# Optimization experiments

Measured on AMD Instinct MI355X. Metric: run time of the kernel, lower is better.

The kernel has to match this reference:

```python
import jax, jax.numpy as jnp
import numpy as np

B, N, D, H = 8, 2048, 512, 8  # batch, seq (incl. CLS), emb_dim, heads


def setup_inputs() -> dict:
    key = jax.random.key(0)
    kx, km, k1, k2, k3, k4 = jax.random.split(key, 6)
    x = jax.random.normal(kx, (B, N, D), dtype=jnp.float32)
    # mask covers the N-1 non-CLS tokens; forward pads a leading True for CLS
    mask = jax.random.bernoulli(km, p=0.9, shape=(B, N - 1))
    s = 0.02
    Wqkv = jax.random.normal(k1, (D, 3 * D), dtype=jnp.float32) * s
    bqkv = jax.random.normal(k2, (3 * D,), dtype=jnp.float32) * s
    Wout = jax.random.normal(k3, (D, D), dtype=jnp.float32) * s
    bout = jax.random.normal(k4, (D,), dtype=jnp.float32) * s
    return {"x": x, "mask": mask, "Wqkv": Wqkv, "bqkv": bqkv,
            "Wout": Wout, "bout": bout, "num_heads": H}


def reference(x, mask, Wqkv, bqkv, Wout, bout, num_heads):
    b, n, d = x.shape
    h = num_heads
    dh = d // h
    scale = d ** (-0.5)  # NOTE: module scales by emb_dim^-0.5, not head_dim^-0.5

    qkv = x @ Wqkv + bqkv                      # [b, n, 3d]
    q, k, v = jnp.split(qkv, 3, axis=-1)
    def to_heads(t):
        return t.reshape(b, n, h, dh).transpose(0, 2, 1, 3)  # [b, h, n, dh]
    q, k, v = map(to_heads, (q, k, v))

    scores = jnp.einsum('bhqd,bhkd->bhqk', q, k) * scale     # [b, h, n, n]

    # pad leading True for CLS token, then outer-product pair mask
    m = jnp.pad(mask, ((0, 0), (1, 0)), constant_values=True)  # [b, n]
    pair = m[:, None, :, None] & m[:, None, None, :]           # [b, 1, n, n]
    neg = jnp.asarray(-1e9, dtype=scores.dtype)  # finite stand-in for -inf (avoids NaN rows)
    scores = jnp.where(pair, scores, neg)

    attn = jax.nn.softmax(scores, axis=-1)
    out = jnp.einsum('bhqk,bhkd->bhqd', attn, v)               # [b, h, n, dh]
    out = out.transpose(0, 2, 1, 3).reshape(b, n, d)
    return out @ Wout + bout
```

## Files before the change

### kernel.cpp

```cpp
#include <hip/hip_runtime.h>
#include <math.h>

#define BB  8
#define SEQ 2048
#define EMB 512
#define NH  8
#define DH  64
#define NBH (BB * NH)
#define MROWS (BB * SEQ)
#define QKV_ELEMS ((size_t)NBH * SEQ * DH)
#define MASK_ELEMS (BB * (SEQ - 1))
#define QSCALE 0.06375871307545f

typedef __attribute__((ext_vector_type(8))) short short8;
typedef __attribute__((ext_vector_type(4))) float float4e;
typedef unsigned short ushort_t;

static __device__ inline unsigned short f2bf(float f) {
    unsigned int u = __float_as_uint(f);
    unsigned int r = (u + 0x7fffu + ((u >> 16) & 1u)) >> 16;
    return (unsigned short)r;
}

static __device__ inline float bf2f(unsigned short h) {
    return __uint_as_float((unsigned int)h << 16);
}

static __device__ inline void gl_lds16(const unsigned short* g, unsigned short* l) {
    __builtin_amdgcn_global_load_lds(
        (const __attribute__((address_space(1))) void*)g,
        (__attribute__((address_space(3))) void*)l, 16, 0, 0);
}

__global__ void decode_mask(const void* __restrict__ mraw, ushort_t* __restrict__ pmh) {
    __shared__ int flag;
    if (threadIdx.x == 0) flag = 0;
    __syncthreads();
    const unsigned int* mi = (const unsigned int*)mraw;
    int local = 0;
    for (int i = threadIdx.x; i < MASK_ELEMS / 4; i += 256) {
        if (mi[i] > 1u) local = 1;
    }
    if (local) flag = 1;
    __syncthreads();
    const int isbyte = flag;
    const unsigned char* mb = (const unsigned char*)mraw;
    const int* m32 = (const int*)mraw;
    for (int i = threadIdx.x; i < BB * SEQ; i += 256) {
        const int b = i >> 11, n = i & (SEQ - 1);
        int v;
        if (n == 0) v = 1;
        else {
            const int src = b * (SEQ - 1) + n - 1;
            v = isbyte ? (int)mb[src] : (m32[src] != 0 ? 1 : 0);
        }
        pmh[i] = v ? 0x3F80 : 0;
    }
}

__global__ __launch_bounds__(256) void conv_x(const float* __restrict__ x,
                                              ushort_t* __restrict__ xb) {
    const size_t i = ((size_t)blockIdx.x * 256 + threadIdx.x) * 4;
    float4 v = *(const float4*)&x[i];
    ushort4 o;
    o.x = f2bf(v.x); o.y = f2bf(v.y); o.z = f2bf(v.z); o.w = f2bf(v.w);
    *(ushort4*)&xb[i] = o;
}

__global__ __launch_bounds__(256) void wtrans(const float* __restrict__ src,
                                              ushort_t* __restrict__ dst,
                                              int K, int N) {
    __shared__ float T[32][33];
    const int tid = threadIdx.x;
    const int n0 = blockIdx.x * 32;
    const int k0 = blockIdx.y * 32;
    {
        const int r = tid >> 3, c4 = (tid & 7) * 4;
        *(float4*)&T[r][c4] = *(const float4*)&src[(size_t)(k0 + r) * N + n0 + c4];
    }
    __syncthreads();
    const int n = tid >> 3, k4 = (tid & 7) * 4;
    ushort4 hv;
    hv.x = f2bf(T[k4 + 0][n]);
    hv.y = f2bf(T[k4 + 1][n]);
    hv.z = f2bf(T[k4 + 2][n]);
    hv.w = f2bf(T[k4 + 3][n]);
    *(ushort4*)&dst[(size_t)(n0 + n) * K + k0 + k4] = hv;
}

__global__ __launch_bounds__(256) void qkv_mfma(const ushort_t* __restrict__ xb,
                                                const ushort_t* __restrict__ wt,
                                                const float* __restrict__ bias,
                                                ushort_t* __restrict__ qb,
                                                ushort_t* __restrict__ kb,
                                                ushort_t* __restrict__ vt) {
    __shared__ __align__(16) ushort_t As[128 * 32];
    __shared__ __align__(16) ushort_t Bs[128 * 32];
    const int tid  = threadIdx.x;
    const int w    = tid >> 6;
    const int lane = tid & 63;
    const int l16  = lane & 15;
    const int quad = lane >> 4;
    const int wq   = w >> 1;
    const int wn   = w & 1;
    const int row0 = blockIdx.y * 128;
    const int col0 = blockIdx.x * 128;

    float4e acc[4][4];
    #pragma unroll
    for (int i = 0; i < 4; ++i)
        #pragma unroll
        for (int j = 0; j < 4; ++j) acc[i][j] = (float4e){0.f, 0.f, 0.f, 0.f};

    const int srow = tid >> 2;
    const int csrc = (tid & 3) ^ (srow & 3);

    for (int k0 = 0; k0 < EMB; k0 += 32) {
        #pragma unroll
        for (int s = 0; s < 2; ++s) {
            const int row = s * 64 + srow;
            gl_lds16(xb + (size_t)(row0 + row) * EMB + k0 + csrc * 8,
                     As + s * 2048 + w * 512);
            gl_lds16(wt + (size_t)(col0 + row) * EMB + k0 + csrc * 8,
                     Bs + s * 2048 + w * 512);
        }
        __syncthreads();
        short8 af[4], bf[4];
        #pragma unroll
        for (int mt = 0; mt < 4; ++mt) {
            const int rm = wq * 64 + mt * 16 + l16;
            af[mt] = *(const short8*)(As + rm * 32 + ((quad ^ (rm & 3)) * 8));
        }
        #pragma unroll
        for (int nt = 0; nt < 4; ++nt) {
            const int rn = wn * 64 + nt * 16 + l16;
            bf[nt] = *(const short8*)(Bs + rn * 32 + ((quad ^ (rn & 3)) * 8));
        }
        #pragma unroll
        for (int mt = 0; mt < 4; ++mt)
            #pragma unroll
            for (int nt = 0; nt < 4; ++nt)
                acc[mt][nt] = __builtin_amdgcn_mfma_f32_16x16x32_bf16(af[mt], bf[nt], acc[mt][nt], 0, 0, 0);
        __syncthreads();
    }

    #pragma unroll
    for (int nt = 0; nt < 4; ++nt) {
        const int cb    = col0 + wn * 64 + nt * 16;
        const int which = cb >> 9;
        const int h     = (cb >> 6) & 7;
        const int dcol  = (cb & 63) + l16;
        const float bz  = bias[cb + l16];
        if (which == 2) {
            #pragma unroll
            for (int mt = 0; mt < 4; ++mt) {
                const int rg = row0 + wq * 64 + mt * 16 + quad * 4;
                const int b = rg >> 11, n = rg & (SEQ - 1);
                ushort4 ov;
                ov.x = f2bf(acc[mt][nt][0] + bz);
                ov.y = f2bf(acc[mt][nt][1] + bz);
                ov.z = f2bf(acc[mt][nt][2] + bz);
                ov.w = f2bf(acc[mt][nt][3] + bz);
                *(ushort4*)&vt[((size_t)(b * NH + h) * DH + dcol) * SEQ + n] = ov;
            }
        } else {
            ushort_t* base = (which == 0) ? qb : kb;
            const float sc = (which == 0) ? QSCALE : 1.0f;
            #pragma unroll
            for (int mt = 0; mt < 4; ++mt) {
                #pragma unroll
                for (int i = 0; i < 4; ++i) {
                    const int rg = row0 + wq * 64 + mt * 16 + quad * 4 + i;
                    const int b = rg >> 11;
                    const int n = rg & (SEQ - 1);
                    base[((size_t)(b * NH + h) * SEQ + n) * DH + dcol] =
                        f2bf((acc[mt][nt][i] + bz) * sc);
                }
            }
        }
    }
}

__global__ __launch_bounds__(256, 4) void attn_mfma(const ushort_t* __restrict__ qb,
                                                    const ushort_t* __restrict__ kb,
                                                    const ushort_t* __restrict__ vt,
                                                    const ushort_t* __restrict__ pmh,
                                                    ushort_t* __restrict__ ab) {
    __shared__ __align__(16) ushort_t Ks[64 * 64];
    __shared__ __align__(16) ushort_t Vts[64 * 64];
    __shared__ __align__(16) ushort_t Ps[4][32 * 64];
    __shared__ ushort_t mskh[SEQ];
    __shared__ float lw[128];

    const int tid  = threadIdx.x;
    const int qt   = blockIdx.x & 15;
    const int bh   = blockIdx.x >> 4;
    const int b    = bh >> 3;
    const int h    = bh & 7;
    const int w    = tid >> 6;
    const int lane = tid & 63;
    const int l16  = lane & 15;
    const int quad = lane >> 4;

    *(short8*)(mskh + tid * 8) = *(const short8*)(pmh + b * SEQ + tid * 8);

    const ushort_t* qbase = qb + ((size_t)bh * SEQ + qt * 128 + w * 32 + l16) * DH;
    short8 qf0[2], qf1[2];
    #pragma unroll
    for (int g = 0; g < 2; ++g) {
        qf0[g] = *(const short8*)(qbase + g * 16 * DH + quad * 8);
        qf1[g] = *(const short8*)(qbase + g * 16 * DH + 32 + quad * 8);
    }

    __syncthreads();

    float mqf[2], fnq[2];
    #pragma unroll
    for (int g = 0; g < 2; ++g) {
        mqf[g] = bf2f(mskh[qt * 128 + w * 32 + g * 16 + l16]);
        fnq[g] = 1.0f - mqf[g];
    }

    float4e o[2][4];
    #pragma unroll
    for (int g = 0; g < 2; ++g)
        #pragma unroll
        for (int d = 0; d < 4; ++d) o[g][d] = (float4e){0.f, 0.f, 0.f, 0.f};
    float l_i[2] = {0.f, 0.f};

    int srow[2], soff[2];
    #pragma unroll
    for (int s = 0; s < 2; ++s) {
        const int c = s * 256 + w * 64 + lane;
        srow[s] = c >> 3;
        soff[s] = ((c & 7) ^ (srow[s] & 7)) * 8;
    }
    const ushort_t* kptr = kb + (size_t)bh * SEQ * DH;
    const ushort_t* vptr = vt + (size_t)bh * DH * SEQ;

    int koff0[4], koff1[4];
    #pragma unroll
    for (int t = 0; t < 4; ++t) {
        const int row = t * 16 + l16;
        koff0[t] = row * 64 + ((quad ^ (row & 7)) * 8);
        koff1[t] = row * 64 + (((4 + quad) ^ (row & 7)) * 8);
    }
    const int psw = (l16 & 7) * 2;
    ushort_t* pwv = &Ps[w][0];
    const int prd0 = ((quad * 2) ^ psw) * 4;
    const int prd1 = (((4 + quad) * 2) ^ psw) * 4;

    for (int kt = 0; kt < 32; ++kt) {
        __syncthreads();
        #pragma unroll
        for (int s = 0; s < 2; ++s) {
            gl_lds16(kptr + (size_t)(kt * 64 + srow[s]) * DH + soff[s],
                     Ks + s * 2048 + w * 512);
            gl_lds16(vptr + (size_t)srow[s] * SEQ + kt * 64 + soff[s],
                     Vts + s * 2048 + w * 512);
        }
        __syncthreads();

        #pragma unroll
        for (int bkb = 0; bkb < 4; ++bkb) {
            const short8 kf0 = *(const short8*)(Ks + koff0[bkb]);
            const short8 kf1 = *(const short8*)(Ks + koff1[bkb]);
            float4e st[2];
            #pragma unroll
            for (int g = 0; g < 2; ++g) {
                st[g] = (float4e){0.f, 0.f, 0.f, 0.f};
                st[g] = __builtin_amdgcn_mfma_f32_16x16x32_bf16(kf0, qf0[g], st[g], 0, 0, 0);
                st[g] = __builtin_amdgcn_mfma_f32_16x16x32_bf16(kf1, qf1[g], st[g], 0, 0, 0);
            }
            const ushort4 mk4 = *(const ushort4*)(mskh + kt * 64 + bkb * 16 + quad * 4);
            const float mkf[4] = {bf2f(mk4.x), bf2f(mk4.y), bf2f(mk4.z), bf2f(mk4.w)};
            const int pc = ((bkb * 4 + quad) ^ psw) * 4;
            #pragma unroll
            for (int g = 0; g < 2; ++g) {
                float p0 = fmaf(__builtin_amdgcn_exp2f(st[g][0]) * mkf[0], mqf[g], fnq[g]);
                float p1 = fmaf(__builtin_amdgcn_exp2f(st[g][1]) * mkf[1], mqf[g], fnq[g]);
                float p2 = fmaf(__builtin_amdgcn_exp2f(st[g][2]) * mkf[2], mqf[g], fnq[g]);
                float p3 = fmaf(__builtin_amdgcn_exp2f(st[g][3]) * mkf[3], mqf[g], fnq[g]);
                l_i[g] += (p0 + p1) + (p2 + p3);
                ushort4 pk;
                pk.x = f2bf(p0); pk.y = f2bf(p1); pk.z = f2bf(p2); pk.w = f2bf(p3);
                *(ushort4*)(pwv + (g * 16 + l16) * 64 + pc) = pk;
            }
        }

        short8 pf0[2], pf1[2];
        #pragma unroll
        for (int g = 0; g < 2; ++g) {
            pf0[g] = *(const short8*)(pwv + (g * 16 + l16) * 64 + prd0);
            pf1[g] = *(const short8*)(pwv + (g * 16 + l16) * 64 + prd1);
        }
        #pragma unroll
        for (int dhb = 0; dhb < 4; ++dhb) {
            const short8 vf0 = *(const short8*)(Vts + koff0[dhb]);
            const short8 vf1 = *(const short8*)(Vts + koff1[dhb]);
            #pragma unroll
            for (int g = 0; g < 2; ++g) {
                o[g][dhb] = __builtin_amdgcn_mfma_f32_16x16x32_bf16(pf0[g], vf0, o[g][dhb], 0, 0, 0);
                o[g][dhb] = __builtin_amdgcn_mfma_f32_16x16x32_bf16(pf1[g], vf1, o[g][dhb], 0, 0, 0);
            }
        }
    }

    #pragma unroll
    for (int g = 0; g < 2; ++g) {
        float l = l_i[g];
        l += __shfl_xor(l, 16);
        l += __shfl_xor(l, 32);
        lw[w * 32 + g * 16 + l16] = l;
    }

    ushort_t* ob = ab + ((size_t)b * SEQ + qt * 128 + w * 32) * EMB + h * DH;
    #pragma unroll
    for (int g = 0; g < 2; ++g) {
        #pragma unroll
        for (int i = 0; i < 4; ++i) {
            const int row = g * 16 + quad * 4 + i;
            const float inv = 1.0f / lw[w * 32 + row];
            #pragma unroll
            for (int dhb = 0; dhb < 4; ++dhb)
                ob[(size_t)row * EMB + dhb * 16 + l16] = f2bf(o[g][dhb][i] * inv);
        }
    }
}

__global__ __launch_bounds__(256) void out_mfma(const ushort_t* __restrict__ ab,
                                                const ushort_t* __restrict__ wot,
                                                const float* __restrict__ bias,
                                                float* __restrict__ out) {
    __shared__ __align__(16) ushort_t As[128 * 32];
    __shared__ __align__(16) ushort_t Bs[128 * 32];
    const int tid  = threadIdx.x;
    const int w    = tid >> 6;
    const int lane = tid & 63;
    const int l16  = lane & 15;
    const int quad = lane >> 4;
    const int wq   = w >> 1;
    const int wn   = w & 1;
    const int row0 = blockIdx.y * 128;
    const int col0 = blockIdx.x * 128;

    float4e acc[4][4];
    #pragma unroll
    for (int i = 0; i < 4; ++i)
        #pragma unroll
        for (int j = 0; j < 4; ++j) acc[i][j] = (float4e){0.f, 0.f, 0.f, 0.f};

    const int srow = tid >> 2;
    const int csrc = (tid & 3) ^ (srow & 3);

    for (int k0 = 0; k0 < EMB; k0 += 32) {
        #pragma unroll
        for (int s = 0; s < 2; ++s) {
            const int row = s * 64 + srow;
            gl_lds16(ab + (size_t)(row0 + row) * EMB + k0 + csrc * 8,
                     As + s * 2048 + w * 512);
            gl_lds16(wot + (size_t)(col0 + row) * EMB + k0 + csrc * 8,
                     Bs + s * 2048 + w * 512);
        }
        __syncthreads();
        short8 af[4], bf[4];
        #pragma unroll
        for (int mt = 0; mt < 4; ++mt) {
            const int rm = wq * 64 + mt * 16 + l16;
            af[mt] = *(const short8*)(As + rm * 32 + ((quad ^ (rm & 3)) * 8));
        }
        #pragma unroll
        for (int nt = 0; nt < 4; ++nt) {
            const int rn = wn * 64 + nt * 16 + l16;
            bf[nt] = *(const short8*)(Bs + rn * 32 + ((quad ^ (rn & 3)) * 8));
        }
        #pragma unroll
        for (int mt = 0; mt < 4; ++mt)
            #pragma unroll
            for (int nt = 0; nt < 4; ++nt)
                acc[mt][nt] = __builtin_amdgcn_mfma_f32_16x16x32_bf16(af[mt], bf[nt], acc[mt][nt], 0, 0, 0);
        __syncthreads();
    }

    #pragma unroll
    for (int nt = 0; nt < 4; ++nt) {
        const int col_g = col0 + wn * 64 + nt * 16 + l16;
        const float bz = bias[col_g];
        #pragma unroll
        for (int mt = 0; mt < 4; ++mt) {
            #pragma unroll
            for (int i = 0; i < 4; ++i) {
                const int row_g = row0 + wq * 64 + mt * 16 + quad * 4 + i;
                out[(size_t)row_g * EMB + col_g] = acc[mt][nt][i] + bz;
            }
        }
    }
}

extern "C" void kernel_launch(void* const* d_in, const int* in_sizes, int n_in,
                              void* d_out, int out_size, void* d_ws, size_t ws_size,
                              hipStream_t stream) {
    const float* x    = (const float*)d_in[0];
    const void*  mask = d_in[1];
    const float* Wqkv = (const float*)d_in[2];
    const float* bqkv = (const float*)d_in[3];
    const float* Wout = (const float*)d_in[4];
    const float* bout = (const float*)d_in[5];
    float* out = (float*)d_out;

    ushort_t* xb  = (ushort_t*)d_ws;
    ushort_t* wqt = xb + (size_t)MROWS * EMB;
    ushort_t* wot = wqt + (size_t)1536 * EMB;
    ushort_t* qb  = wot + (size_t)EMB * EMB;
    ushort_t* kb  = qb + QKV_ELEMS;
    ushort_t* vt  = kb + QKV_ELEMS;
    ushort_t* ab  = vt + QKV_ELEMS;
    ushort_t* pmh = ab + (size_t)MROWS * EMB;

    decode_mask<<<1, 256, 0, stream>>>(mask, pmh);
    conv_x<<<dim3(MROWS * EMB / 1024), 256, 0, stream>>>(x, xb);
    wtrans<<<dim3(1536 / 32, EMB / 32), 256, 0, stream>>>(Wqkv, wqt, EMB, 1536);
    wtrans<<<dim3(EMB / 32, EMB / 32), 256, 0, stream>>>(Wout, wot, EMB, EMB);
    qkv_mfma<<<dim3(1536 / 128, MROWS / 128), 256, 0, stream>>>(xb, wqt, bqkv, qb, kb, vt);
    attn_mfma<<<dim3(NBH * (SEQ / 128)), 256, 0, stream>>>(qb, kb, vt, pmh, ab);
    out_mfma<<<dim3(EMB / 128, MROWS / 128), 256, 0, stream>>>(ab, wot, bout, out);
}
```

Measured before the change: 285.9 us.

## Enlarge attention query tile, read K/V directly from global, truncate P to bf16

The attention kernel now gives each wave 64 query rows instead of 32 and handles 256 queries per block, so each K/V fragment feeds more MFMAs. It drops the shared-memory staging of K and V and the two block-wide barriers per key tile, loading the fragments straight from global memory and relying on cache. P is packed to bf16 by truncation instead of round-to-nearest, and the masked-query blend is replaced by a select. Separately, decode_mask now runs across 64 blocks instead of one. The trade-offs are higher register pressure (launch bounds lowered to 2), fewer blocks, uncoalesced global fragment loads, and slightly less accurate P.

```diff
diff --git a/kernel.cpp b/kernel.cpp
--- a/kernel.cpp
+++ b/kernel.cpp
@@ -26,13 +26,18 @@
     return __uint_as_float((unsigned int)h << 16);
 }
 
+static __device__ inline unsigned int pk_bf_trunc(float a, float b) {
+    return (__float_as_uint(a) >> 16) | (__float_as_uint(b) & 0xffff0000u);
+}
+
 static __device__ inline void gl_lds16(const unsigned short* g, unsigned short* l) {
     __builtin_amdgcn_global_load_lds(
         (const __attribute__((address_space(1))) void*)g,
         (__attribute__((address_space(3))) void*)l, 16, 0, 0);
 }
 
-__global__ void decode_mask(const void* __restrict__ mraw, ushort_t* __restrict__ pmh) {
+__global__ __launch_bounds__(256) void decode_mask(const void* __restrict__ mraw,
+                                                   ushort_t* __restrict__ pmh) {
     __shared__ int flag;
     if (threadIdx.x == 0) flag = 0;
     __syncthreads();
@@ -46,16 +51,15 @@
     const int isbyte = flag;
     const unsigned char* mb = (const unsigned char*)mraw;
     const int* m32 = (const int*)mraw;
-    for (int i = threadIdx.x; i < BB * SEQ; i += 256) {
-        const int b = i >> 11, n = i & (SEQ - 1);
-        int v;
-        if (n == 0) v = 1;
-        else {
-            const int src = b * (SEQ - 1) + n - 1;
-            v = isbyte ? (int)mb[src] : (m32[src] != 0 ? 1 : 0);
-        }
-        pmh[i] = v ? 0x3F80 : 0;
-    }
+    const int i = blockIdx.x * 256 + threadIdx.x;
+    const int b = i >> 11, n = i & (SEQ - 1);
+    int v;
+    if (n == 0) v = 1;
+    else {
+        const int src = b * (SEQ - 1) + n - 1;
+        v = isbyte ? (int)mb[src] : (m32[src] != 0 ? 1 : 0);
+    }
+    pmh[i] = v ? 0x3F80 : 0;
 }
 
 __global__ __launch_bounds__(256) void conv_x(const float* __restrict__ x,
@@ -181,20 +185,18 @@
     }
 }
 
-__global__ __launch_bounds__(256, 4) void attn_mfma(const ushort_t* __restrict__ qb,
+__global__ __launch_bounds__(256, 2) void attn_mfma(const ushort_t* __restrict__ qb,
                                                     const ushort_t* __restrict__ kb,
                                                     const ushort_t* __restrict__ vt,
                                                     const ushort_t* __restrict__ pmh,
                                                     ushort_t* __restrict__ ab) {
-    __shared__ __align__(16) ushort_t Ks[64 * 64];
-    __shared__ __align__(16) ushort_t Vts[64 * 64];
-    __shared__ __align__(16) ushort_t Ps[4][32 * 64];
+    __shared__ __align__(16) ushort_t Ps[4][64 * 64];
     __shared__ ushort_t mskh[SEQ];
-    __shared__ float lw[128];
+    __shared__ float lw[4][64];
 
     const int tid  = threadIdx.x;
-    const int qt   = blockIdx.x & 15;
-    const int bh   = blockIdx.x >> 4;
+    const int qt   = blockIdx.x & 7;
+    const int bh   = blockIdx.x >> 3;
     const int b    = bh >> 3;
     const int h    = bh & 7;
     const int w    = tid >> 6;
@@ -204,123 +206,109 @@
 
     *(short8*)(mskh + tid * 8) = *(const short8*)(pmh + b * SEQ + tid * 8);
 
-    const ushort_t* qbase = qb + ((size_t)bh * SEQ + qt * 128 + w * 32 + l16) * DH;
-    short8 qf0[2], qf1[2];
-    #pragma unroll
-    for (int g = 0; g < 2; ++g) {
+    const int q0 = qt * 256 + w * 64;
+
+    const ushort_t* qbase = qb + ((size_t)bh * SEQ + q0 + l16) * DH;
+    short8 qf0[4], qf1[4];
+    #pragma unroll
+    for (int g = 0; g < 4; ++g) {
         qf0[g] = *(const short8*)(qbase + g * 16 * DH + quad * 8);
         qf1[g] = *(const short8*)(qbase + g * 16 * DH + 32 + quad * 8);
     }
 
     __syncthreads();
 
-    float mqf[2], fnq[2];
-    #pragma unroll
-    for (int g = 0; g < 2; ++g) {
-        mqf[g] = bf2f(mskh[qt * 128 + w * 32 + g * 16 + l16]);
-        fnq[g] = 1.0f - mqf[g];
-    }
-
-    float4e o[2][4];
-    #pragma unroll
-    for (int g = 0; g < 2; ++g)
+    bool bq[4];
+    #pragma unroll
+    for (int g = 0; g < 4; ++g)
+        bq[g] = bf2f(mskh[q0 + g * 16 + l16]) > 0.5f;
+
+    float4e o[4][4];
+    #pragma unroll
+    for (int g = 0; g < 4; ++g)
         #pragma unroll
         for (int d = 0; d < 4; ++d) o[g][d] = (float4e){0.f, 0.f, 0.f, 0.f};
-    float l_i[2] = {0.f, 0.f};
-
-    int srow[2], soff[2];
-    #pragma unroll
-    for (int s = 0; s < 2; ++s) {
-        const int c = s * 256 + w * 64 + lane;
-        srow[s] = c >> 3;
-        soff[s] = ((c & 7) ^ (srow[s] & 7)) * 8;
-    }
-    const ushort_t* kptr = kb + (size_t)bh * SEQ * DH;
-    const ushort_t* vptr = vt + (size_t)bh * DH * SEQ;
-
-    int koff0[4], koff1[4];
-    #pragma unroll
-    for (int t = 0; t < 4; ++t) {
-        const int row = t * 16 + l16;
-        koff0[t] = row * 64 + ((quad ^ (row & 7)) * 8);
-        koff1[t] = row * 64 + (((4 + quad) ^ (row & 7)) * 8);
-    }
-    const int psw = (l16 & 7) * 2;
-    ushort_t* pwv = &Ps[w][0];
-    const int prd0 = ((quad * 2) ^ psw) * 4;
-    const int prd1 = (((4 + quad) * 2) ^ psw) * 4;
+    float l_i[4] = {0.f, 0.f, 0.f, 0.f};
+
+    const ushort_t* kbh = kb + (size_t)bh * SEQ * DH;
+    const ushort_t* vbh = vt + (size_t)bh * DH * SEQ;
+
+    char* Pw = (char*)&Ps[w][0];
+    const int hsw = l16 & 7;
+    int pcB[4], prB[2];
+    #pragma unroll
+    for (int bkb = 0; bkb < 4; ++bkb)
+        pcB[bkb] = (((2 * bkb + (quad >> 1)) ^ hsw) * 16) + ((quad & 1) * 8);
+    #pragma unroll
+    for (int kc = 0; kc < 2; ++kc)
+        prB[kc] = ((kc * 4 + quad) ^ hsw) * 16;
 
     for (int kt = 0; kt < 32; ++kt) {
-        __syncthreads();
-        #pragma unroll
-        for (int s = 0; s < 2; ++s) {
-            gl_lds16(kptr + (size_t)(kt * 64 + srow[s]) * DH + soff[s],
-                     Ks + s * 2048 + w * 512);
-            gl_lds16(vptr + (size_t)srow[s] * SEQ + kt * 64 + soff[s],
-                     Vts + s * 2048 + w * 512);
-        }
-        __syncthreads();
+        const ushort_t* kB = kbh + (size_t)kt * 64 * DH;
+        const ushort_t* vB = vbh + kt * 64;
 
         #pragma unroll
         for (int bkb = 0; bkb < 4; ++bkb) {
-            const short8 kf0 = *(const short8*)(Ks + koff0[bkb]);
-            const short8 kf1 = *(const short8*)(Ks + koff1[bkb]);
-            float4e st[2];
-            #pragma unroll
-            for (int g = 0; g < 2; ++g) {
+            const ushort_t* krow = kB + (size_t)(bkb * 16 + l16) * DH + quad * 8;
+            const short8 kf0 = *(const short8*)(krow);
+            const short8 kf1 = *(const short8*)(krow + 32);
+            float4e st[4];
+            #pragma unroll
+            for (int g = 0; g < 4; ++g) {
                 st[g] = (float4e){0.f, 0.f, 0.f, 0.f};
                 st[g] = __builtin_amdgcn_mfma_f32_16x16x32_bf16(kf0, qf0[g], st[g], 0, 0, 0);
                 st[g] = __builtin_amdgcn_mfma_f32_16x16x32_bf16(kf1, qf1[g], st[g], 0, 0, 0);
             }
             const ushort4 mk4 = *(const ushort4*)(mskh + kt * 64 + bkb * 16 + quad * 4);
             const float mkf[4] = {bf2f(mk4.x), bf2f(mk4.y), bf2f(mk4.z), bf2f(mk4.w)};
-            const int pc = ((bkb * 4 + quad) ^ psw) * 4;
-            #pragma unroll
-            for (int g = 0; g < 2; ++g) {
-                float p0 = fmaf(__builtin_amdgcn_exp2f(st[g][0]) * mkf[0], mqf[g], fnq[g]);
-                float p1 = fmaf(__builtin_amdgcn_exp2f(st[g][1]) * mkf[1], mqf[g], fnq[g]);
-                float p2 = fmaf(__builtin_amdgcn_exp2f(st[g][2]) * mkf[2], mqf[g], fnq[g]);
-                float p3 = fmaf(__builtin_amdgcn_exp2f(st[g][3]) * mkf[3], mqf[g], fnq[g]);
+            #pragma unroll
+            for (int g = 0; g < 4; ++g) {
+                const float p0 = bq[g] ? __builtin_amdgcn_exp2f(st[g][0]) * mkf[0] : 1.0f;
+                const float p1 = bq[g] ? __builtin_amdgcn_exp2f(st[g][1]) * mkf[1] : 1.0f;
+                const float p2 = bq[g] ? __builtin_amdgcn_exp2f(st[g][2]) * mkf[2] : 1.0f;
+                const float p3 = bq[g] ? __builtin_amdgcn_exp2f(st[g][3]) * mkf[3] : 1.0f;
                 l_i[g] += (p0 + p1) + (p2 + p3);
-                ushort4 pk;
-                pk.x = f2bf(p0); pk.y = f2bf(p1); pk.z = f2bf(p2); pk.w = f2bf(p3);
-                *(ushort4*)(pwv + (g * 16 + l16) * 64 + pc) = pk;
-            }
-        }
-
-        short8 pf0[2], pf1[2];
-        #pragma unroll
-        for (int g = 0; g < 2; ++g) {
-            pf0[g] = *(const short8*)(pwv + (g * 16 + l16) * 64 + prd0);
-            pf1[g] = *(const short8*)(pwv + (g * 16 + l16) * 64 + prd1);
-        }
+                uint2 pk;
+                pk.x = pk_bf_trunc(p0, p1);
+                pk.y = pk_bf_trunc(p2, p3);
+                *(uint2*)(Pw + (g * 16 + l16) * 128 + pcB[bkb]) = pk;
+            }
+        }
+
+        short8 pf[4][2];
+        #pragma unroll
+        for (int g = 0; g < 4; ++g)
+            #pragma unroll
+            for (int kc = 0; kc < 2; ++kc)
+                pf[g][kc] = *(const short8*)(Pw + (g * 16 + l16) * 128 + prB[kc]);
         #pragma unroll
         for (int dhb = 0; dhb < 4; ++dhb) {
-            const short8 vf0 = *(const short8*)(Vts + koff0[dhb]);
-            const short8 vf1 = *(const short8*)(Vts + koff1[dhb]);
-            #pragma unroll
-            for (int g = 0; g < 2; ++g) {
-                o[g][dhb] = __builtin_amdgcn_mfma_f32_16x16x32_bf16(pf0[g], vf0, o[g][dhb], 0, 0, 0);
-                o[g][dhb] = __builtin_amdgcn_mfma_f32_16x16x32_bf16(pf1[g], vf1, o[g][dhb], 0, 0, 0);
-            }
-        }
-    }
-
-    #pragma unroll
-    for (int g = 0; g < 2; ++g) {
+            const ushort_t* vrow = vB + (size_t)(dhb * 16 + l16) * SEQ + quad * 8;
+            #pragma unroll
+            for (int kc = 0; kc < 2; ++kc) {
+                const short8 vf = *(const short8*)(vrow + kc * 32);
+                #pragma unroll
+                for (int g = 0; g < 4; ++g)
+                    o[g][dhb] = __builtin_amdgcn_mfma_f32_16x16x32_bf16(pf[g][kc], vf, o[g][dhb], 0, 0, 0);
+            }
+        }
+    }
+
+    #pragma unroll
+    for (int g = 0; g < 4; ++g) {
         float l = l_i[g];
         l += __shfl_xor(l, 16);
         l += __shfl_xor(l, 32);
-        lw[w * 32 + g * 16 + l16] = l;
-    }
-
-    ushort_t* ob = ab + ((size_t)b * SEQ + qt * 128 + w * 32) * EMB + h * DH;
-    #pragma unroll
-    for (int g = 0; g < 2; ++g) {
+        lw[w][g * 16 + l16] = l;
+    }
+
+    ushort_t* ob = ab + ((size_t)b * SEQ + q0) * EMB + h * DH;
+    #pragma unroll
+    for (int g = 0; g < 4; ++g) {
         #pragma unroll
         for (int i = 0; i < 4; ++i) {
             const int row = g * 16 + quad * 4 + i;
-            const float inv = 1.0f / lw[w * 32 + row];
+            const float inv = 1.0f / lw[w][row];
             #pragma unroll
             for (int dhb = 0; dhb < 4; ++dhb)
                 ob[(size_t)row * EMB + dhb * 16 + l16] = f2bf(o[g][dhb][i] * inv);
@@ -417,11 +405,11 @@
     ushort_t* ab  = vt + QKV_ELEMS;
     ushort_t* pmh = ab + (size_t)MROWS * EMB;
 
-    decode_mask<<<1, 256, 0, stream>>>(mask, pmh);
+    decode_mask<<<dim3(64), 256, 0, stream>>>(mask, pmh);
     conv_x<<<dim3(MROWS * EMB / 1024), 256, 0, stream>>>(x, xb);
     wtrans<<<dim3(1536 / 32, EMB / 32), 256, 0, stream>>>(Wqkv, wqt, EMB, 1536);
     wtrans<<<dim3(EMB / 32, EMB / 32), 256, 0, stream>>>(Wout, wot, EMB, EMB);
     qkv_mfma<<<dim3(1536 / 128, MROWS / 128), 256, 0, stream>>>(xb, wqt, bqkv, qb, kb, vt);
-    attn_mfma<<<dim3(NBH * (SEQ / 128)), 256, 0, stream>>>(qb, kb, vt, pmh, ab);
+    attn_mfma<<<dim3(NBH * (SEQ / 256)), 256, 0, stream>>>(qb, kb, vt, pmh, ab);
     out_mfma<<<dim3(EMB / 128, MROWS / 128), 256, 0, stream>>>(ab, wot, bout, out);
 }
```

Measured after the change: 289.0 us. Within noise of the previous version (+1.1%).

## Fuse prep kernels into one launch and register-prefetch K/V tiles in attention

Applied to the files above, without the earlier changes.

Merges mask decoding, x conversion and both weight transposes into a single prep kernel, and spreads the mask decode across 64 blocks. This removes three launches and the serial single-block mask pass. Each mask block still rescans the whole mask to detect the byte format, so that scan now runs 64 times. The attention kernel no longer uses direct global-to-LDS loads. It prefetches the next K/V tile into registers while the current tile is being computed, then stores it to swizzled LDS. This trades extra register pressure for overlap of global memory latency with compute. It also reads the query mask straight from global memory, which drops one barrier.

```diff
diff --git a/kernel.cpp b/kernel.cpp
--- a/kernel.cpp
+++ b/kernel.cpp
@@ -32,21 +32,44 @@
         (__attribute__((address_space(3))) void*)l, 16, 0, 0);
 }
 
-__global__ void decode_mask(const void* __restrict__ mraw, ushort_t* __restrict__ pmh) {
+#define PREP_CONV   8192
+#define PREP_MASK   (PREP_CONV + 64)
+#define PREP_WQ     (PREP_MASK + (1536 / 32) * (EMB / 32))
+#define PREP_TOTAL  (PREP_WQ + (EMB / 32) * (EMB / 32))
+
+__global__ __launch_bounds__(256) void prep(const float* __restrict__ x,
+                                            const void* __restrict__ mraw,
+                                            const float* __restrict__ Wqkv,
+                                            const float* __restrict__ Wout,
+                                            ushort_t* __restrict__ xb,
+                                            ushort_t* __restrict__ pmh,
+                                            ushort_t* __restrict__ wqt,
+                                            ushort_t* __restrict__ wot) {
+    __shared__ float T[32][33];
     __shared__ int flag;
-    if (threadIdx.x == 0) flag = 0;
-    __syncthreads();
-    const unsigned int* mi = (const unsigned int*)mraw;
-    int local = 0;
-    for (int i = threadIdx.x; i < MASK_ELEMS / 4; i += 256) {
-        if (mi[i] > 1u) local = 1;
-    }
-    if (local) flag = 1;
-    __syncthreads();
-    const int isbyte = flag;
-    const unsigned char* mb = (const unsigned char*)mraw;
-    const int* m32 = (const int*)mraw;
-    for (int i = threadIdx.x; i < BB * SEQ; i += 256) {
+    const int bid = blockIdx.x;
+    const int tid = threadIdx.x;
+
+    if (bid < PREP_CONV) {
+        const size_t i = ((size_t)bid * 256 + tid) * 4;
+        float4 v = *(const float4*)&x[i];
+        ushort4 o;
+        o.x = f2bf(v.x); o.y = f2bf(v.y); o.z = f2bf(v.z); o.w = f2bf(v.w);
+        *(ushort4*)&xb[i] = o;
+    } else if (bid < PREP_MASK) {
+        if (tid == 0) flag = 0;
+        __syncthreads();
+        const unsigned int* mi = (const unsigned int*)mraw;
+        int local = 0;
+        for (int i = tid; i < MASK_ELEMS / 4; i += 256) {
+            if (mi[i] > 1u) local = 1;
+        }
+        if (local) flag = 1;
+        __syncthreads();
+        const int isbyte = flag;
+        const unsigned char* mb = (const unsigned char*)mraw;
+        const int* m32 = (const int*)mraw;
+        const int i = (bid - PREP_CONV) * 256 + tid;
         const int b = i >> 11, n = i & (SEQ - 1);
         int v;
         if (n == 0) v = 1;
@@ -55,37 +78,31 @@
             v = isbyte ? (int)mb[src] : (m32[src] != 0 ? 1 : 0);
         }
         pmh[i] = v ? 0x3F80 : 0;
-    }
-}
-
-__global__ __launch_bounds__(256) void conv_x(const float* __restrict__ x,
-                                              ushort_t* __restrict__ xb) {
-    const size_t i = ((size_t)blockIdx.x * 256 + threadIdx.x) * 4;
-    float4 v = *(const float4*)&x[i];
-    ushort4 o;
-    o.x = f2bf(v.x); o.y = f2bf(v.y); o.z = f2bf(v.z); o.w = f2bf(v.w);
-    *(ushort4*)&xb[i] = o;
-}
-
-__global__ __launch_bounds__(256) void wtrans(const float* __restrict__ src,
-                                              ushort_t* __restrict__ dst,
-                                              int K, int N) {
-    __shared__ float T[32][33];
-    const int tid = threadIdx.x;
-    const int n0 = blockIdx.x * 32;
-    const int k0 = blockIdx.y * 32;
-    {
-        const int r = tid >> 3, c4 = (tid & 7) * 4;
-        *(float4*)&T[r][c4] = *(const float4*)&src[(size_t)(k0 + r) * N + n0 + c4];
-    }
-    __syncthreads();
-    const int n = tid >> 3, k4 = (tid & 7) * 4;
-    ushort4 hv;
-    hv.x = f2bf(T[k4 + 0][n]);
-    hv.y = f2bf(T[k4 + 1][n]);
-    hv.z = f2bf(T[k4 + 2][n]);
-    hv.w = f2bf(T[k4 + 3][n]);
-    *(ushort4*)&dst[(size_t)(n0 + n) * K + k0 + k4] = hv;
+    } else {
+        const float* src;
+        ushort_t* dst;
+        int N, idx;
+        if (bid < PREP_WQ) {
+            src = Wqkv; dst = wqt; N = 1536; idx = bid - PREP_MASK;
+        } else {
+            src = Wout; dst = wot; N = EMB; idx = bid - PREP_WQ;
+        }
+        const int nb = N / 32;
+        const int n0 = (idx % nb) * 32;
+        const int k0 = (idx / nb) * 32;
+        {
+            const int r = tid >> 3, c4 = (tid & 7) * 4;
+            *(float4*)&T[r][c4] = *(const float4*)&src[(size_t)(k0 + r) * N + n0 + c4];
+        }
+        __syncthreads();
+        const int n = tid >> 3, k4 = (tid & 7) * 4;
+        ushort4 hv;
+        hv.x = f2bf(T[k4 + 0][n]);
+        hv.y = f2bf(T[k4 + 1][n]);
+        hv.z = f2bf(T[k4 + 2][n]);
+        hv.w = f2bf(T[k4 + 3][n]);
+        *(ushort4*)&dst[(size_t)(n0 + n) * EMB + k0 + k4] = hv;
+    }
 }
 
 __global__ __launch_bounds__(256) void qkv_mfma(const ushort_t* __restrict__ xb,
@@ -212,12 +229,10 @@
         qf1[g] = *(const short8*)(qbase + g * 16 * DH + 32 + quad * 8);
     }
 
-    __syncthreads();
-
     float mqf[2], fnq[2];
     #pragma unroll
     for (int g = 0; g < 2; ++g) {
-        mqf[g] = bf2f(mskh[qt * 128 + w * 32 + g * 16 + l16]);
+        mqf[g] = bf2f(pmh[b * SEQ + qt * 128 + w * 32 + g * 16 + l16]);
         fnq[g] = 1.0f - mqf[g];
     }
 
@@ -228,12 +243,13 @@
         for (int d = 0; d < 4; ++d) o[g][d] = (float4e){0.f, 0.f, 0.f, 0.f};
     float l_i[2] = {0.f, 0.f};
 
-    int srow[2], soff[2];
+    int crow[2], ccol[2], cdst[2];
     #pragma unroll
     for (int s = 0; s < 2; ++s) {
-        const int c = s * 256 + w * 64 + lane;
-        srow[s] = c >> 3;
-        soff[s] = ((c & 7) ^ (srow[s] & 7)) * 8;
+        const int c = s * 256 + tid;
+        crow[s] = c >> 3;
+        ccol[s] = (c & 7) * 8;
+        cdst[s] = crow[s] * 64 + (((c & 7) ^ (crow[s] & 7)) * 8);
     }
     const ushort_t* kptr = kb + (size_t)bh * SEQ * DH;
     const ushort_t* vptr = vt + (size_t)bh * DH * SEQ;
@@ -250,16 +266,29 @@
     const int prd0 = ((quad * 2) ^ psw) * 4;
     const int prd1 = (((4 + quad) * 2) ^ psw) * 4;
 
+    short8 kreg[2], vreg[2];
+    #pragma unroll
+    for (int s = 0; s < 2; ++s) {
+        kreg[s] = *(const short8*)(kptr + (size_t)crow[s] * DH + ccol[s]);
+        vreg[s] = *(const short8*)(vptr + (size_t)crow[s] * SEQ + ccol[s]);
+    }
+
     for (int kt = 0; kt < 32; ++kt) {
         __syncthreads();
         #pragma unroll
         for (int s = 0; s < 2; ++s) {
-            gl_lds16(kptr + (size_t)(kt * 64 + srow[s]) * DH + soff[s],
-                     Ks + s * 2048 + w * 512);
-            gl_lds16(vptr + (size_t)srow[s] * SEQ + kt * 64 + soff[s],
-                     Vts + s * 2048 + w * 512);
-        }
-        __syncthreads();
+            *(short8*)(Ks + cdst[s])  = kreg[s];
+            *(short8*)(Vts + cdst[s]) = vreg[s];
+        }
+        __syncthreads();
+
+        if (kt < 31) {
+            #pragma unroll
+            for (int s = 0; s < 2; ++s) {
+                kreg[s] = *(const short8*)(kptr + (size_t)((kt + 1) * 64 + crow[s]) * DH + ccol[s]);
+                vreg[s] = *(const short8*)(vptr + (size_t)crow[s] * SEQ + (kt + 1) * 64 + ccol[s]);
+            }
+        }
 
         #pragma unroll
         for (int bkb = 0; bkb < 4; ++bkb) {
@@ -417,10 +446,7 @@
     ushort_t* ab  = vt + QKV_ELEMS;
     ushort_t* pmh = ab + (size_t)MROWS * EMB;
 
-    decode_mask<<<1, 256, 0, stream>>>(mask, pmh);
-    conv_x<<<dim3(MROWS * EMB / 1024), 256, 0, stream>>>(x, xb);
-    wtrans<<<dim3(1536 / 32, EMB / 32), 256, 0, stream>>>(Wqkv, wqt, EMB, 1536);
-    wtrans<<<dim3(EMB / 32, EMB / 32), 256, 0, stream>>>(Wout, wot, EMB, EMB);
+    prep<<<dim3(PREP_TOTAL), 256, 0, stream>>>(x, mask, Wqkv, Wout, xb, pmh, wqt, wot);
     qkv_mfma<<<dim3(1536 / 128, MROWS / 128), 256, 0, stream>>>(xb, wqt, bqkv, qb, kb, vt);
     attn_mfma<<<dim3(NBH * (SEQ / 128)), 256, 0, stream>>>(qb, kb, vt, pmh, ab);
     out_mfma<<<dim3(EMB / 128, MROWS / 128), 256, 0, stream>>>(ab, wot, bout, out);
```

Measured after the change: 280.0 us. 2.1% less time.
